# Optimization experiments

Hardware: AMD Instinct MI355X
Metric: run time of the kernel (lower is better)

The kernel has to match this reference:

```python
import jax, jax.numpy as jnp
import numpy as np

TINY = 1e-13  # tiny_value_of_dtype(float32)


def gru_cell(x, h, Wx, Wh, bx, bh):
    gx = x @ Wx + bx
    gh = h @ Wh + bh
    xr, xz, xn = jnp.split(gx, 3, -1)
    hr, hz, hn = jnp.split(gh, 3, -1)
    r = jax.nn.sigmoid(xr + hr)
    z = jax.nn.sigmoid(xz + hz)
    n = jnp.tanh(xn + r * hn)
    return (1.0 - z) * n + z * h


def setup_inputs() -> dict:
    B, V, VT, D, OPT, SEQ, SRC = 256, 2000, 10000, 256, 16, 10, 40
    key = jax.random.key(0)
    ks = jax.random.split(key, 20)
    rn = lambda i, shape, s: jax.random.normal(ks[i], shape, jnp.float32) * s
    inp = {}
    inp['lhs'] = jax.random.randint(ks[0], (B,), 0, V)
    inp['lhs_mask'] = jnp.ones((B,), jnp.int32)
    inp['tree_state'] = rn(1, (B, D), 1.0)
    sym = jax.random.randint(ks[2], (B, OPT, SEQ), 0, V)
    pg = jax.random.randint(ks[3], (B, OPT, SEQ), 0, 2)
    fg = jax.random.randint(ks[4], (B, OPT, SEQ), 0, 2)
    lens = jax.random.randint(ks[5], (B, OPT), 1, SEQ + 1)
    msk = (jnp.arange(SEQ)[None, None, :] < lens[:, :, None]).astype(jnp.int32)
    inp['grammar_guide'] = jnp.stack([sym, pg, fg, msk], axis=2)  # (B,OPT,4,SEQ)
    inp['emb'] = rn(6, (V, D), 0.02)
    inp['mem'] = rn(7, (B, SRC, D), 1.0)  # encoder memory for query_attn_fn
    inp['Wx'] = rn(8, (D, 3 * D), 0.05)
    inp['Wh'] = rn(9, (D, 3 * D), 0.05)
    inp['bx'] = jnp.zeros((3 * D,), jnp.float32)
    inp['bh'] = jnp.zeros((3 * D,), jnp.float32)
    inp['Wc'] = rn(10, (2 * D, D), 0.05)
    inp['bc'] = jnp.zeros((D,), jnp.float32)
    inp['Wsym'] = rn(11, (D, V), 0.05)
    inp['bsym'] = jnp.zeros((V,), jnp.float32)
    inp['Wtok'] = rn(12, (2 * D, VT), 0.05)
    inp['btok'] = jnp.zeros((VT,), jnp.float32)
    inp['tok_table'] = (jax.random.uniform(ks[13], (V, VT)) < 0.05).astype(jnp.float32)
    return inp


def reference(lhs, lhs_mask, tree_state, grammar_guide, emb, mem, Wx, Wh, bx, bh,
              Wc, bc, Wsym, bsym, Wtok, btok, tok_table):
    B, OPT, _, SEQ = grammar_guide.shape
    V = emb.shape[0]
    D = emb.shape[1]
    g_sym = grammar_guide[:, :, 0, :]   # (B,OPT,SEQ) symbol options
    g_mask = grammar_guide[:, :, 3, :]  # (B,OPT,SEQ) option mask

    def step_fn(carry, xs):
        step_inp, ts = carry
        opts, omask = xs  # (B,OPT) ints
        x = emb[step_inp]                      # embedding (dropout = identity, eval mode)
        # hx re-initialized each step from the fixed pre-step tree state
        h = gru_cell(x, tree_state, Wx, Wh, bx, bh)  # (B,D) step_out
        att = jax.nn.softmax(jnp.einsum('bd,bsd->bs', h, mem), axis=-1)
        ctx = jnp.einsum('bs,bsd->bd', att, mem)
        step_out_att = jnp.tanh(jnp.concatenate([ctx, h], -1) @ Wc + bc)
        logits = step_out_att @ Wsym + bsym    # (B,V)
        ts_new = jnp.tanh(ts + step_out_att)   # tree state updater
        # grammar compliance masking
        comp = opts * omask                    # (B,OPT)
        w = jnp.sum(jax.nn.one_hot(comp, V, dtype=jnp.float32), axis=1) > 0  # (B,V) bool
        w0 = jnp.sum((comp == 0) * omask, axis=-1) > 0
        w = w.at[:, 0].set(w0)
        clogits = logits + jnp.log(w.astype(logits.dtype) + TINY)
        nxt = jnp.argmax(clogits, axis=-1)     # free-running next input
        return (nxt, ts_new), clogits

    xs = (jnp.moveaxis(g_sym, -1, 0), jnp.moveaxis(g_mask, -1, 0))  # (SEQ,B,OPT)
    (_, ts_final), seq_logits = jax.lax.scan(step_fn, (lhs, tree_state), xs)
    seq_logits = jnp.moveaxis(seq_logits, 0, -1)                 # (B,V,SEQ)
    seq_logp = jnp.log(jax.nn.softmax(seq_logits, axis=1) + TINY)
    seq_opts_logp = jnp.take_along_axis(seq_logp, g_sym, axis=1)  # (B,OPT,SEQ)
    opts_logp = jnp.sum(seq_opts_logp * g_mask, axis=-1)          # (B,OPT)

    # tree topology inference: pick best option row of grammar_guide
    best = jnp.argmax(opts_logp, axis=-1)
    topo = jnp.take_along_axis(grammar_guide, best[:, None, None, None], axis=1)[:, 0]  # (B,4,SEQ)
    symbol, p_growth, f_growth, mask = topo[:, 0], topo[:, 1], topo[:, 2], topo[:, 3]

    # exact token prediction after derivation
    cw = tok_table[symbol]                     # (B,SEQ,VT) token compliance
    s_emb = emb[symbol]                        # (B,SEQ,D)
    ts_tiled = jnp.broadcast_to(ts_final[:, None, :], (B, SEQ, D))
    proj = jnp.concatenate([s_emb, ts_tiled], axis=-1)
    exact_logit = proj @ Wtok + btok + jnp.log(cw + TINY)  # (B,SEQ,VT)

    return (lhs, lhs_mask, grammar_guide, opts_logp,
            (symbol, p_growth, f_growth, mask), exact_logit)
```

## Files before the change

kernel.cpp:

```cpp
#include <hip/hip_runtime.h>
#include <math.h>

#define BB 256
#define DD 256
#define VV 2000
#define VT 10000
#define OPTN 16
#define SEQN 10
#define SRCN 40
#define D3 768
#define D2 512

#define LOG_TINY (-29.9336062f)

#define OFF_OPTS  (2*BB + BB*OPTN*4*SEQN)
#define OFF_TOPO  (OFF_OPTS + BB*OPTN)
#define OFF_EXACT (OFF_TOPO + 4*BB*SEQN)

#define TOKB_STRIDE 320
#define TOKB_W 313

#define NWG_TOK 1580

typedef __bf16 bf16x8 __attribute__((ext_vector_type(8)));
typedef float  f32x4  __attribute__((ext_vector_type(4)));

__device__ __forceinline__ float sigm(float x){ return 1.0f/(1.0f+expf(-x)); }
__device__ __forceinline__ unsigned short f2bf(float x){
  union { float f; unsigned int u; } v; v.f = x;
  unsigned int r = (v.u + 0x7FFF + ((v.u >> 16) & 1)) >> 16;
  return (unsigned short)r;
}

__global__ void k_gh(const float* __restrict__ ts0, const float* __restrict__ Wh,
                     const float* __restrict__ bh, float* __restrict__ gh){
  int b = blockIdx.x;
  int j = blockIdx.y*256 + threadIdx.x;
  __shared__ float hsh[DD];
  hsh[threadIdx.x] = ts0[b*DD + threadIdx.x];
  __syncthreads();
  float a0 = bh[j], a1 = 0.f, a2 = 0.f, a3 = 0.f;
  #pragma unroll 4
  for(int k=0;k<DD;k+=4){
    a0 = fmaf(hsh[k+0], Wh[(k+0)*D3 + j], a0);
    a1 = fmaf(hsh[k+1], Wh[(k+1)*D3 + j], a1);
    a2 = fmaf(hsh[k+2], Wh[(k+2)*D3 + j], a2);
    a3 = fmaf(hsh[k+3], Wh[(k+3)*D3 + j], a3);
  }
  gh[b*D3 + j] = (a0+a1)+(a2+a3);
}

__global__ void k_ew(const float* __restrict__ emb, const float* __restrict__ Wx,
                     float* __restrict__ EW){
  __shared__ float As[16][64];
  __shared__ float Bs[16][64];
  int tid = threadIdx.x;
  int tx = tid & 15, ty = tid >> 4;
  int m0 = blockIdx.y*64, n0 = blockIdx.x*64;
  float acc[4][4];
  #pragma unroll
  for(int i=0;i<4;i++){ acc[i][0]=0.f; acc[i][1]=0.f; acc[i][2]=0.f; acc[i][3]=0.f; }
  for(int k0=0;k0<DD;k0+=16){
    {
      int row = tid >> 2, kk = (tid & 3)*4;
      int m = m0 + row;
      float4 av = {0,0,0,0};
      if(m < VV) av = *(const float4*)&emb[m*DD + k0 + kk];
      As[kk+0][row]=av.x; As[kk+1][row]=av.y; As[kk+2][row]=av.z; As[kk+3][row]=av.w;
    }
    {
      int r = tid >> 4, c2 = (tid & 15)*4;
      float4 bv = *(const float4*)&Wx[(k0+r)*D3 + n0 + c2];
      *(float4*)&Bs[r][c2] = bv;
    }
    __syncthreads();
    #pragma unroll
    for(int k=0;k<16;k++){
      float4 a4 = *(const float4*)&As[k][ty*4];
      float4 b4 = *(const float4*)&Bs[k][tx*4];
      float av[4] = {a4.x,a4.y,a4.z,a4.w};
      float bw[4] = {b4.x,b4.y,b4.z,b4.w};
      #pragma unroll
      for(int i=0;i<4;i++)
        #pragma unroll
        for(int j=0;j<4;j++) acc[i][j] = fmaf(av[i], bw[j], acc[i][j]);
    }
    __syncthreads();
  }
  #pragma unroll
  for(int i=0;i<4;i++){
    int m = m0 + ty*4 + i;
    if(m < VV){
      #pragma unroll
      for(int j=0;j<4;j++) EW[m*D3 + n0 + tx*4 + j] = acc[i][j];
    }
  }
}

__global__ void k_wtokT(const float* __restrict__ Wtok, unsigned short* __restrict__ WtokB){
  __shared__ float tile[32][65];
  int tid = threadIdx.x;
  int n0 = blockIdx.x*64, k0 = blockIdx.y*32;
  #pragma unroll
  for(int p=0;p<8;p++){
    int idx = tid + p*256;
    int kk = idx >> 6, nn = idx & 63;
    int n = n0 + nn;
    tile[kk][nn] = (n < VT) ? Wtok[(size_t)(k0+kk)*VT + n] : 0.f;
  }
  __syncthreads();
  #pragma unroll
  for(int p=0;p<4;p++){
    int idx = tid + p*256;
    int nn = idx >> 4, kk = (idx & 15)*2;
    int n = n0 + nn;
    if(n < VT){
      ushort2 v;
      v.x = f2bf(tile[kk][nn]);
      v.y = f2bf(tile[kk+1][nn]);
      *(ushort2*)&WtokB[(size_t)n*D2 + k0 + kk] = v;
    }
  }
}

__global__ __launch_bounds__(256) void k_tokbits(const float* __restrict__ tok_table,
                                                 unsigned int* __restrict__ bits){
  int idx = blockIdx.x*256 + threadIdx.x;
  const int total = VV*TOKB_W;
  for(; idx < total; idx += gridDim.x*256){
    int v = idx / TOKB_W, w = idx - v*TOKB_W;
    const float* row = tok_table + (size_t)v*VT + w*32;
    unsigned int bv = 0;
    if(w*32 + 32 <= VT){
      #pragma unroll
      for(int k=0;k<8;k++){
        float4 x = *(const float4*)(row + k*4);
        bv |= (x.x>0.5f?1u:0u) << (k*4+0);
        bv |= (x.y>0.5f?1u:0u) << (k*4+1);
        bv |= (x.z>0.5f?1u:0u) << (k*4+2);
        bv |= (x.w>0.5f?1u:0u) << (k*4+3);
      }
    } else {
      for(int k=0;k<32;k++){
        int n = w*32 + k;
        if(n < VT && row[k] > 0.5f) bv |= 1u << k;
      }
    }
    bits[v*TOKB_STRIDE + w] = bv;
  }
}

__global__ __launch_bounds__(512) void k_chain(
    const int* __restrict__ lhs, const float* __restrict__ EW,
    const float* __restrict__ gh, const float* __restrict__ bx,
    const float* __restrict__ tree_state, const float* __restrict__ mem,
    const float* __restrict__ Wc, const float* __restrict__ bc,
    const float* __restrict__ Wsym, const float* __restrict__ bsym,
    const int* __restrict__ gg, float* __restrict__ cl,
    float* __restrict__ ts){
  int b = blockIdx.x, tid = threadIdx.x;
  int lane = tid & 63, wv = tid >> 6;
  __shared__ float memsh[SRCN][DD];
  __shared__ float bsymsh[VV];
  __shared__ float bxsh[D3];
  __shared__ float ghsh[D3];
  __shared__ float bcsh[DD];
  __shared__ float tssh[DD];
  __shared__ float hsh[DD], csh[DD], soash[DD];
  __shared__ float psum[2][DD];
  __shared__ float sc[SRCN];
  __shared__ unsigned int selw[64];
  __shared__ int symsh;
  __shared__ float wmax[8]; __shared__ int widx[8];

  for(int i = tid; i < SRCN*DD; i += 512) ((float*)memsh)[i] = mem[(size_t)b*SRCN*DD + i];
  for(int i = tid; i < VV; i += 512) bsymsh[i] = bsym[i];
  for(int i = tid; i < D3; i += 512){ bxsh[i] = bx[i]; ghsh[i] = gh[(size_t)b*D3 + i]; }
  if(tid < DD){ bcsh[tid] = bc[tid]; tssh[tid] = tree_state[b*DD + tid]; }
  float t0 = (tid < DD) ? tree_state[b*DD + tid] : 0.f;
  if(tid == 0) symsh = lhs[b];
  __syncthreads();

  for(int t = 0; t < SEQN; t++){
    int sym = symsh;
    if(tid < 64) selw[tid] = 0u;
    __syncthreads();
    if(tid < OPTN){
      int base = ((b*OPTN + tid)*4)*SEQN + t;
      int mk = gg[base + 3*SEQN];
      int v = mk ? gg[base] : -1;
      if(v >= 0) atomicOr(&selw[v>>5], 1u << (v&31));
    }
    if(tid < DD){
      const float* ew = EW + (size_t)sym*D3;
      float r = sigm(ew[tid]     + bxsh[tid]     + ghsh[tid]);
      float z = sigm(ew[256+tid] + bxsh[256+tid] + ghsh[256+tid]);
      float n = tanhf(ew[512+tid] + bxsh[512+tid] + r*ghsh[512+tid]);
      hsh[tid] = (1.0f - z)*n + z*t0;
    }
    __syncthreads();
    for(int s = wv; s < SRCN; s += 8){
      float p = 0.f;
      #pragma unroll 4
      for(int d = lane; d < DD; d += 64) p = fmaf(hsh[d], memsh[s][d], p);
      for(int off=32; off; off>>=1) p += __shfl_down(p, off, 64);
      if(lane == 0) sc[s] = p;
    }
    __syncthreads();
    if(tid < 64){
      float v = (tid < SRCN) ? sc[tid] : -1e30f;
      float mx = v;
      for(int off=32; off; off>>=1) mx = fmaxf(mx, __shfl_xor(mx, off, 64));
      float e = (tid < SRCN) ? expf(v - mx) : 0.f;
      float su = e;
      for(int off=32; off; off>>=1) su += __shfl_xor(su, off, 64);
      if(tid < SRCN) sc[tid] = e / su;
    }
    __syncthreads();
    if(tid < DD){
      float c = 0.f;
      #pragma unroll 8
      for(int s=0;s<SRCN;s++) c = fmaf(sc[s], memsh[s][tid], c);
      csh[tid] = c;
    }
    __syncthreads();
    {
      int j = tid & 255, half = tid >> 8;
      const float* src = half ? hsh : csh;
      const float* w = Wc + (size_t)half*256*DD + j;
      float a0=0.f, a1=0.f, a2=0.f, a3=0.f;
      #pragma unroll 4
      for(int k=0;k<256;k+=4){
        a0 = fmaf(src[k+0], w[(size_t)(k+0)*DD], a0);
        a1 = fmaf(src[k+1], w[(size_t)(k+1)*DD], a1);
        a2 = fmaf(src[k+2], w[(size_t)(k+2)*DD], a2);
        a3 = fmaf(src[k+3], w[(size_t)(k+3)*DD], a3);
      }
      psum[half][j] = (a0+a1)+(a2+a3);
    }
    __syncthreads();
    if(tid < DD){
      float sv = tanhf(psum[0][tid] + psum[1][tid] + bcsh[tid]);
      soash[tid] = sv;
      tssh[tid] = tanhf(tssh[tid] + sv);
    }
    __syncthreads();
    float bv = -3.0e30f; int bn = 0x7FFFFFFF;
    if(tid < 500){
      int c0 = tid*4;
      const float* wcol = Wsym + c0;
      float4 a = {0.f,0.f,0.f,0.f};
      #pragma unroll 8
      for(int k=0;k<DD;k++){
        float sk = soash[k];
        float4 w4 = *(const float4*)(wcol + (size_t)k*VV);
        a.x = fmaf(sk, w4.x, a.x);
        a.y = fmaf(sk, w4.y, a.y);
        a.z = fmaf(sk, w4.z, a.z);
        a.w = fmaf(sk, w4.w, a.w);
      }
      float vals[4];
      #pragma unroll
      for(int j=0;j<4;j++){
        int n = c0 + j;
        unsigned int wb = selw[n >> 5];
        vals[j] = ((float*)&a)[j] + bsymsh[n] + (((wb >> (n&31)) & 1u) ? 0.f : LOG_TINY);
      }
      float4 o; o.x=vals[0]; o.y=vals[1]; o.z=vals[2]; o.w=vals[3];
      *(float4*)&cl[((size_t)t*BB + b)*VV + c0] = o;
      #pragma unroll
      for(int j=0;j<4;j++){
        if(vals[j] > bv){ bv = vals[j]; bn = c0 + j; }
      }
    }
    #pragma unroll
    for(int off=1; off<64; off<<=1){
      float ov = __shfl_xor(bv, off, 64);
      int   on = __shfl_xor(bn, off, 64);
      if(ov > bv || (ov == bv && on < bn)){ bv = ov; bn = on; }
    }
    if(lane == 0){ wmax[wv] = bv; widx[wv] = bn; }
    __syncthreads();
    if(tid == 0){
      float m = wmax[0]; int mi = widx[0];
      #pragma unroll
      for(int w=1; w<8; w++)
        if(wmax[w] > m || (wmax[w] == m && widx[w] < mi)){ m = wmax[w]; mi = widx[w]; }
      symsh = mi;
    }
    __syncthreads();
  }
  if(tid < DD) ts[b*DD + tid] = tssh[tid];
}

__global__ void k_opts(const float* __restrict__ cl, const int* __restrict__ gg,
                       const float* __restrict__ emb, const float* __restrict__ ts,
                       float* __restrict__ out, int* __restrict__ sym_i,
                       unsigned short* __restrict__ A){
  int b = blockIdx.x, tid = threadIdx.x;
  int lane = tid & 63, wv = tid >> 6;
  __shared__ float redm[4], reds[4];
  __shared__ float lse_sh[SEQN];
  __shared__ float sacc[OPTN];
  __shared__ int ssym[SEQN];
  __shared__ int sbest;
  for(int t=0;t<SEQN;t++){
    const float* row = cl + ((size_t)t*BB + b)*VV;
    float mx = -1e30f;
    for(int v=tid; v<VV; v+=256) mx = fmaxf(mx, row[v]);
    for(int off=32; off; off>>=1) mx = fmaxf(mx, __shfl_xor(mx, off, 64));
    if(lane==0) redm[wv] = mx;
    __syncthreads();
    float gmx = fmaxf(fmaxf(redm[0],redm[1]), fmaxf(redm[2],redm[3]));
    float sum = 0.f;
    for(int v=tid; v<VV; v+=256) sum += expf(row[v]-gmx);
    for(int off=32; off; off>>=1) sum += __shfl_xor(sum, off, 64);
    if(lane==0) reds[wv] = sum;
    __syncthreads();
    if(tid==0) lse_sh[t] = gmx + logf(reds[0]+reds[1]+reds[2]+reds[3]);
    __syncthreads();
  }
  if(tid < OPTN){
    int o = tid;
    float acc = 0.f;
    for(int t=0;t<SEQN;t++){
      int base = ((b*OPTN + o)*4)*SEQN + t;
      int mk = gg[base + 3*SEQN];
      if(mk){
        int v = gg[base];
        float p = expf(cl[((size_t)t*BB + b)*VV + v] - lse_sh[t]);
        acc += logf(p + 1e-13f);
      }
    }
    sacc[o] = acc;
    out[OFF_OPTS + b*OPTN + o] = acc;
  }
  __syncthreads();
  if(tid==0){
    float mx = sacc[0]; int mi = 0;
    for(int o=1;o<OPTN;o++) if(sacc[o] > mx){ mx = sacc[o]; mi = o; }
    sbest = mi;
  }
  __syncthreads();
  if(tid < 4*SEQN){
    int c = tid/SEQN, t = tid%SEQN;
    int val = gg[((b*OPTN + sbest)*4 + c)*SEQN + t];
    out[OFF_TOPO + c*(BB*SEQN) + b*SEQN + t] = (float)val;
    if(c==0){ sym_i[b*SEQN + t] = val; ssym[t] = val; }
  }
  __syncthreads();
  for(int idx = tid; idx < SEQN*D2; idx += 256){
    int t = idx >> 9, k = idx & 511;
    float val = (k < DD) ? emb[ssym[t]*DD + k] : ts[b*DD + (k-DD)];
    A[(size_t)(b*SEQN + t)*D2 + k] = f2bf(val);
  }
}

__global__ void k_pass(const int* __restrict__ lhs, const int* __restrict__ lhs_mask,
                       const int* __restrict__ gg, float* __restrict__ out){
  int i = blockIdx.x*256 + threadIdx.x;
  if(i < BB) out[i] = (float)lhs[i];
  else if(i < 2*BB) out[i] = (float)lhs_mask[i - BB];
  else if(i < 2*BB + BB*OPTN*4*SEQN) out[2*BB + (i - 2*BB)] = (float)gg[i - 2*BB];
}

__global__ __launch_bounds__(256) void k_tok_mfma(
    const unsigned short* __restrict__ A, const unsigned short* __restrict__ Bw,
    const float* __restrict__ btok, const unsigned int* __restrict__ tokbits,
    const int* __restrict__ sym_i, float* __restrict__ out){
  __shared__ __align__(16) unsigned short Ssh[4*5120];
  __shared__ float sBtok[128];
  int tid = threadIdx.x;
  int lane = tid & 63, wave = tid >> 6;
  int c = lane & 15, q = lane >> 4;
  int wm = (wave >> 1)*64, wn = (wave & 1)*64;

  int id = blockIdx.x;
  int xcd = id & 7, off = id >> 3;
  const int qq = NWG_TOK >> 3, rr = NWG_TOK & 7;
  int start = (xcd < rr) ? xcd*(qq+1) : rr*(qq+1) + (xcd-rr)*qq;
  int ord = start + off;
  int mb = ord % 20, nb = ord / 20;
  int m0 = mb*128, n0 = nb*128;

  if(tid < 128){
    int n = n0 + tid;
    sBtok[tid] = (n < VT) ? btok[n] : 0.f;
  }
  f32x4 acc[4][4];
  #pragma unroll
  for(int i=0;i<4;i++)
    #pragma unroll
    for(int j=0;j<4;j++) acc[i][j] = (f32x4){0.f,0.f,0.f,0.f};

  int arow = tid >> 2;
  int ach  = (tid & 3) * 8;
  const size_t aoff0 = (size_t)(m0 + arow)*D2 + ach;
  const size_t aoff1 = (size_t)(m0 + 64 + arow)*D2 + ach;
  int bn0 = n0 + arow, bn1 = n0 + 64 + arow;
  bool b0ok = bn0 < VT, b1ok = bn1 < VT;
  const size_t boff0 = (size_t)bn0*D2 + ach;
  const size_t boff1 = (size_t)bn1*D2 + ach;
  const float4 f0 = {0.f,0.f,0.f,0.f};

  float4 ra0 = *(const float4*)(A + aoff0);
  float4 ra1 = *(const float4*)(A + aoff1);
  float4 rb0 = b0ok ? *(const float4*)(Bw + boff0) : f0;
  float4 rb1 = b1ok ? *(const float4*)(Bw + boff1) : f0;

  for(int t=0; t<16; t++){
    unsigned short* As = Ssh + (t&1)*10240;
    unsigned short* Bs = As + 5120;
    *(float4*)(As + arow*40 + ach)      = ra0;
    *(float4*)(As + (64+arow)*40 + ach) = ra1;
    *(float4*)(Bs + arow*40 + ach)      = rb0;
    *(float4*)(Bs + (64+arow)*40 + ach) = rb1;
    __syncthreads();
    if(t < 15){
      int k0 = (t+1)*32;
      ra0 = *(const float4*)(A + aoff0 + k0);
      ra1 = *(const float4*)(A + aoff1 + k0);
      if(b0ok) rb0 = *(const float4*)(Bw + boff0 + k0);
      if(b1ok) rb1 = *(const float4*)(Bw + boff1 + k0);
    }
    bf16x8 af[4], bf[4];
    #pragma unroll
    for(int i=0;i<4;i++) af[i] = *(const bf16x8*)(As + (wm + i*16 + c)*40 + q*8);
    #pragma unroll
    for(int j=0;j<4;j++) bf[j] = *(const bf16x8*)(Bs + (wn + j*16 + c)*40 + q*8);
    #pragma unroll
    for(int i=0;i<4;i++)
      #pragma unroll
      for(int j=0;j<4;j++)
        acc[i][j] = __builtin_amdgcn_mfma_f32_16x16x32_bf16(af[i], bf[j], acc[i][j], 0, 0, 0);
  }
  __syncthreads();

  float* sw = (float*)Ssh + wave*(64*21);
  int lrow = lane >> 2, ln4 = lane & 3;
  #pragma unroll
  for(int i=0;i<4;i++){
    #pragma unroll
    for(int j=0;j<4;j++){
      int col = j*16 + c;
      #pragma unroll
      for(int r2=0;r2<4;r2++) sw[col*21 + q*4 + r2] = acc[i][j][r2];
    }
    int row_g = m0 + wm + i*16 + lrow;
    int s = sym_i[row_g];
    const unsigned int* bt = tokbits + (size_t)s*TOKB_STRIDE;
    float* orow = out + OFF_EXACT + (size_t)row_g*VT;
    #pragma unroll
    for(int s4=0;s4<4;s4++){
      int colo = ln4*4 + s4*16;
      int n = n0 + wn + colo;
      if(n < VT){
        float4 bt4 = *(const float4*)&sBtok[wn + colo];
        unsigned int wb = bt[n >> 5];
        int sh = n & 31;
        float4 o;
        o.x = sw[(colo+0)*21 + lrow] + bt4.x + (((wb>>(sh+0))&1u) ? 0.f : LOG_TINY);
        o.y = sw[(colo+1)*21 + lrow] + bt4.y + (((wb>>(sh+1))&1u) ? 0.f : LOG_TINY);
        o.z = sw[(colo+2)*21 + lrow] + bt4.z + (((wb>>(sh+2))&1u) ? 0.f : LOG_TINY);
        o.w = sw[(colo+3)*21 + lrow] + bt4.w + (((wb>>(sh+3))&1u) ? 0.f : LOG_TINY);
        *(float4*)(orow + n) = o;
      }
    }
  }
}

extern "C" void kernel_launch(void* const* d_in, const int* in_sizes, int n_in,
                              void* d_out, int out_size, void* d_ws, size_t ws_size,
                              hipStream_t stream) {
  const int*   lhs       = (const int*)  d_in[0];
  const int*   lhs_mask  = (const int*)  d_in[1];
  const float* tree_state= (const float*)d_in[2];
  const int*   gg        = (const int*)  d_in[3];
  const float* emb       = (const float*)d_in[4];
  const float* mem       = (const float*)d_in[5];
  const float* Wx        = (const float*)d_in[6];
  const float* Wh        = (const float*)d_in[7];
  const float* bx        = (const float*)d_in[8];
  const float* bh        = (const float*)d_in[9];
  const float* Wc        = (const float*)d_in[10];
  const float* bc        = (const float*)d_in[11];
  const float* Wsym      = (const float*)d_in[12];
  const float* bsym      = (const float*)d_in[13];
  const float* Wtok      = (const float*)d_in[14];
  const float* btok      = (const float*)d_in[15];
  const float* tok_table = (const float*)d_in[16];
  float* out = (float*)d_out;

  float* W    = (float*)d_ws;
  float* gh   = W;
  float* ts   = gh  + BB*D3;
  float* cl   = ts  + BB*DD;
  float* EW   = cl  + (size_t)SEQN*BB*VV;
  int*   sym_i= (int*)(EW + VV*D3);
  unsigned short* Abf  = (unsigned short*)(sym_i + BB*SEQN);
  unsigned short* WtokB= Abf + (size_t)BB*SEQN*D2;
  unsigned int* tokbits= (unsigned int*)(WtokB + (size_t)VT*D2);

  k_pass<<<(2*BB + BB*OPTN*4*SEQN + 255)/256, 256, 0, stream>>>(lhs, lhs_mask, gg, out);
  k_tokbits<<<2048, 256, 0, stream>>>(tok_table, tokbits);
  k_wtokT<<<dim3((VT+63)/64, D2/32), 256, 0, stream>>>(Wtok, WtokB);
  k_gh<<<dim3(BB,3), 256, 0, stream>>>(tree_state, Wh, bh, gh);
  k_ew<<<dim3(D3/64, (VV+63)/64), 256, 0, stream>>>(emb, Wx, EW);

  k_chain<<<BB, 512, 0, stream>>>(lhs, EW, gh, bx, tree_state, mem, Wc, bc,
                                  Wsym, bsym, gg, cl, ts);

  k_opts<<<BB, 256, 0, stream>>>(cl, gg, emb, ts, out, sym_i, Abf);
  k_tok_mfma<<<NWG_TOK, 256, 0, stream>>>(Abf, WtokB, btok, tokbits, sym_i, out);
}
```

Baseline: 633.4 us.

## Restrict per-step argmax to candidate symbols and batch symbol logits into a tiled GEMM

Inside the sequential chain kernel, the next symbol is now chosen by computing logits only for the up-to-16 allowed option symbols. Non-candidates always carry a log-tiny penalty, so they cannot win while any candidate exists. The full 2000-column Wsym projection per step is skipped unless no candidate is present. The per-step attention outputs are stored, and the full logits are computed afterwards in one tiled GEMM kernel, with the masking fused in and log-sum-exp moved into its own parallel kernel. This takes the large serialized matvec off the critical sequential path, at the cost of extra launches and an extra round trip through memory.

New measurement: 569.9 us. 1.11x faster.

```diff
diff --git a/kernel.cpp b/kernel.cpp
--- a/kernel.cpp
+++ b/kernel.cpp
@@ -156,12 +156,11 @@
     const float* __restrict__ tree_state, const float* __restrict__ mem,
     const float* __restrict__ Wc, const float* __restrict__ bc,
     const float* __restrict__ Wsym, const float* __restrict__ bsym,
-    const int* __restrict__ gg, float* __restrict__ cl,
+    const int* __restrict__ gg, float* __restrict__ soa_all,
     float* __restrict__ ts){
   int b = blockIdx.x, tid = threadIdx.x;
   int lane = tid & 63, wv = tid >> 6;
   __shared__ float memsh[SRCN][DD];
-  __shared__ float bsymsh[VV];
   __shared__ float bxsh[D3];
   __shared__ float ghsh[D3];
   __shared__ float bcsh[DD];
@@ -169,12 +168,12 @@
   __shared__ float hsh[DD], csh[DD], soash[DD];
   __shared__ float psum[2][DD];
   __shared__ float sc[SRCN];
-  __shared__ unsigned int selw[64];
+  __shared__ int cvs[16];
+  __shared__ float cvals[16];
   __shared__ int symsh;
   __shared__ float wmax[8]; __shared__ int widx[8];
 
   for(int i = tid; i < SRCN*DD; i += 512) ((float*)memsh)[i] = mem[(size_t)b*SRCN*DD + i];
-  for(int i = tid; i < VV; i += 512) bsymsh[i] = bsym[i];
   for(int i = tid; i < D3; i += 512){ bxsh[i] = bx[i]; ghsh[i] = gh[(size_t)b*D3 + i]; }
   if(tid < DD){ bcsh[tid] = bc[tid]; tssh[tid] = tree_state[b*DD + tid]; }
   float t0 = (tid < DD) ? tree_state[b*DD + tid] : 0.f;
@@ -183,13 +182,10 @@
 
   for(int t = 0; t < SEQN; t++){
     int sym = symsh;
-    if(tid < 64) selw[tid] = 0u;
-    __syncthreads();
-    if(tid < OPTN){
+    if(tid < 16){
       int base = ((b*OPTN + tid)*4)*SEQN + t;
       int mk = gg[base + 3*SEQN];
-      int v = mk ? gg[base] : -1;
-      if(v >= 0) atomicOr(&selw[v>>5], 1u << (v&31));
+      cvs[tid] = mk ? gg[base] : -1;
     }
     if(tid < DD){
       const float* ew = EW + (size_t)sym*D3;
@@ -242,84 +238,199 @@
     if(tid < DD){
       float sv = tanhf(psum[0][tid] + psum[1][tid] + bcsh[tid]);
       soash[tid] = sv;
+      soa_all[(size_t)(t*BB + b)*DD + tid] = sv;
       tssh[tid] = tanhf(tssh[tid] + sv);
     }
     __syncthreads();
-    float bv = -3.0e30f; int bn = 0x7FFFFFFF;
-    if(tid < 500){
-      int c0 = tid*4;
-      const float* wcol = Wsym + c0;
-      float4 a = {0.f,0.f,0.f,0.f};
-      #pragma unroll 8
-      for(int k=0;k<DD;k++){
-        float sk = soash[k];
-        float4 w4 = *(const float4*)(wcol + (size_t)k*VV);
-        a.x = fmaf(sk, w4.x, a.x);
-        a.y = fmaf(sk, w4.y, a.y);
-        a.z = fmaf(sk, w4.z, a.z);
-        a.w = fmaf(sk, w4.w, a.w);
-      }
-      float vals[4];
+    bool anyc = false;
+    #pragma unroll
+    for(int i=0;i<16;i++) anyc |= (cvs[i] >= 0);
+    if(anyc){
+      if(tid < 256){
+        int g = tid >> 4, l = tid & 15;
+        int v = cvs[g];
+        float d = 0.f;
+        if(v >= 0){
+          #pragma unroll
+          for(int k=0;k<16;k++) d = fmaf(soash[l*16+k], Wsym[(size_t)(l*16+k)*VV + v], d);
+        }
+        d += __shfl_xor(d, 1, 64); d += __shfl_xor(d, 2, 64);
+        d += __shfl_xor(d, 4, 64); d += __shfl_xor(d, 8, 64);
+        if(l == 0) cvals[g] = (v >= 0) ? d + bsym[v] : -3.0e30f;
+      }
+      __syncthreads();
+      if(tid == 0){
+        float bvv = -3.0e30f; int bnn = 0x7FFFFFFF;
+        #pragma unroll
+        for(int g=0; g<16; g++){
+          int v = cvs[g];
+          if(v >= 0){
+            float val = cvals[g];
+            if(val > bvv || (val == bvv && v < bnn)){ bvv = val; bnn = v; }
+          }
+        }
+        symsh = bnn;
+      }
+      __syncthreads();
+    } else {
+      float bv = -3.0e30f; int bn = 0x7FFFFFFF;
+      if(tid < 500){
+        int c0 = tid*4;
+        const float* wcol = Wsym + c0;
+        float4 a = {0.f,0.f,0.f,0.f};
+        #pragma unroll 8
+        for(int k=0;k<DD;k++){
+          float sk = soash[k];
+          float4 w4 = *(const float4*)(wcol + (size_t)k*VV);
+          a.x = fmaf(sk, w4.x, a.x);
+          a.y = fmaf(sk, w4.y, a.y);
+          a.z = fmaf(sk, w4.z, a.z);
+          a.w = fmaf(sk, w4.w, a.w);
+        }
+        #pragma unroll
+        for(int j=0;j<4;j++){
+          int n = c0 + j;
+          float val = ((float*)&a)[j] + bsym[n] + LOG_TINY;
+          if(val > bv){ bv = val; bn = n; }
+        }
+      }
+      #pragma unroll
+      for(int off=1; off<64; off<<=1){
+        float ov = __shfl_xor(bv, off, 64);
+        int   on = __shfl_xor(bn, off, 64);
+        if(ov > bv || (ov == bv && on < bn)){ bv = ov; bn = on; }
+      }
+      if(lane == 0){ wmax[wv] = bv; widx[wv] = bn; }
+      __syncthreads();
+      if(tid == 0){
+        float m = wmax[0]; int mi = widx[0];
+        #pragma unroll
+        for(int w=1; w<8; w++)
+          if(wmax[w] > m || (wmax[w] == m && widx[w] < mi)){ m = wmax[w]; mi = widx[w]; }
+        symsh = mi;
+      }
+      __syncthreads();
+    }
+  }
+  if(tid < DD) ts[b*DD + tid] = tssh[tid];
+}
+
+__global__ void k_cl(const float* __restrict__ A, const float* __restrict__ Wsym,
+                     const float* __restrict__ bsym, const int* __restrict__ gg,
+                     float* __restrict__ cl){
+  __shared__ float As[16][32];
+  __shared__ float Bs[16][64];
+  __shared__ unsigned int selb[32][2];
+  int tid = threadIdx.x;
+  int tx = tid & 15, ty = tid >> 4;
+  int m0 = blockIdx.y*32, n0 = blockIdx.x*64;
+  if(tid < 64) selb[tid>>1][tid&1] = 0u;
+  __syncthreads();
+  for(int idx = tid; idx < 32*OPTN; idx += 256){
+    int i = idx >> 4, o = idx & 15;
+    int m = m0 + i;
+    int bb = m & (BB-1), t = m >> 8;
+    int base = ((bb*OPTN + o)*4)*SEQN + t;
+    int mk = gg[base + 3*SEQN];
+    int v = mk ? gg[base] : -1;
+    unsigned int d = (unsigned int)(v - n0);
+    if(d < 64u) atomicOr(&selb[i][d>>5], 1u << (d&31));
+  }
+  float acc[2][4];
+  #pragma unroll
+  for(int i=0;i<2;i++){ acc[i][0]=0.f; acc[i][1]=0.f; acc[i][2]=0.f; acc[i][3]=0.f; }
+  for(int k0=0;k0<DD;k0+=16){
+    if(tid < 128){
+      int row = tid >> 2, kk = (tid & 3)*4;
+      float4 av = *(const float4*)&A[(size_t)(m0+row)*DD + k0 + kk];
+      As[kk+0][row]=av.x; As[kk+1][row]=av.y; As[kk+2][row]=av.z; As[kk+3][row]=av.w;
+    }
+    {
+      int r = tid >> 4, c2 = (tid & 15)*4;
+      int n = n0 + c2;
+      float4 bv;
+      if(n + 3 < VV){ bv = *(const float4*)&Wsym[(k0+r)*VV + n]; }
+      else {
+        bv.x = (n+0<VV)? Wsym[(k0+r)*VV + n+0] : 0.f;
+        bv.y = (n+1<VV)? Wsym[(k0+r)*VV + n+1] : 0.f;
+        bv.z = (n+2<VV)? Wsym[(k0+r)*VV + n+2] : 0.f;
+        bv.w = (n+3<VV)? Wsym[(k0+r)*VV + n+3] : 0.f;
+      }
+      *(float4*)&Bs[r][c2] = bv;
+    }
+    __syncthreads();
+    #pragma unroll
+    for(int k=0;k<16;k++){
+      float a0 = As[k][ty*2+0];
+      float a1 = As[k][ty*2+1];
+      float4 b4 = *(const float4*)&Bs[k][tx*4];
+      acc[0][0] = fmaf(a0, b4.x, acc[0][0]);
+      acc[0][1] = fmaf(a0, b4.y, acc[0][1]);
+      acc[0][2] = fmaf(a0, b4.z, acc[0][2]);
+      acc[0][3] = fmaf(a0, b4.w, acc[0][3]);
+      acc[1][0] = fmaf(a1, b4.x, acc[1][0]);
+      acc[1][1] = fmaf(a1, b4.y, acc[1][1]);
+      acc[1][2] = fmaf(a1, b4.z, acc[1][2]);
+      acc[1][3] = fmaf(a1, b4.w, acc[1][3]);
+    }
+    __syncthreads();
+  }
+  #pragma unroll
+  for(int i=0;i<2;i++){
+    int m = m0 + ty*2 + i;
+    unsigned int s0 = selb[ty*2+i][0], s1 = selb[ty*2+i][1];
+    float vals[4];
+    #pragma unroll
+    for(int j=0;j<4;j++){
+      int n = n0 + tx*4 + j;
+      int nn = tx*4 + j;
+      unsigned int wb = (nn < 32) ? s0 : s1;
+      vals[j] = acc[i][j] + ((n < VV) ? bsym[n] : 0.f) + (((wb >> (nn&31)) & 1u) ? 0.f : LOG_TINY);
+    }
+    int nb = n0 + tx*4;
+    if(nb + 3 < VV){
+      float4 o; o.x=vals[0]; o.y=vals[1]; o.z=vals[2]; o.w=vals[3];
+      *(float4*)&cl[(size_t)m*VV + nb] = o;
+    } else {
       #pragma unroll
       for(int j=0;j<4;j++){
-        int n = c0 + j;
-        unsigned int wb = selw[n >> 5];
-        vals[j] = ((float*)&a)[j] + bsymsh[n] + (((wb >> (n&31)) & 1u) ? 0.f : LOG_TINY);
-      }
-      float4 o; o.x=vals[0]; o.y=vals[1]; o.z=vals[2]; o.w=vals[3];
-      *(float4*)&cl[((size_t)t*BB + b)*VV + c0] = o;
-      #pragma unroll
-      for(int j=0;j<4;j++){
-        if(vals[j] > bv){ bv = vals[j]; bn = c0 + j; }
-      }
-    }
-    #pragma unroll
-    for(int off=1; off<64; off<<=1){
-      float ov = __shfl_xor(bv, off, 64);
-      int   on = __shfl_xor(bn, off, 64);
-      if(ov > bv || (ov == bv && on < bn)){ bv = ov; bn = on; }
-    }
-    if(lane == 0){ wmax[wv] = bv; widx[wv] = bn; }
-    __syncthreads();
-    if(tid == 0){
-      float m = wmax[0]; int mi = widx[0];
-      #pragma unroll
-      for(int w=1; w<8; w++)
-        if(wmax[w] > m || (wmax[w] == m && widx[w] < mi)){ m = wmax[w]; mi = widx[w]; }
-      symsh = mi;
-    }
-    __syncthreads();
-  }
-  if(tid < DD) ts[b*DD + tid] = tssh[tid];
-}
-
-__global__ void k_opts(const float* __restrict__ cl, const int* __restrict__ gg,
-                       const float* __restrict__ emb, const float* __restrict__ ts,
-                       float* __restrict__ out, int* __restrict__ sym_i,
-                       unsigned short* __restrict__ A){
+        int n = nb + j;
+        if(n < VV) cl[(size_t)m*VV + n] = vals[j];
+      }
+    }
+  }
+}
+
+__global__ void k_lse(const float* __restrict__ cl, float* __restrict__ lse_g){
+  int m = blockIdx.x;
+  int tid = threadIdx.x, lane = tid & 63, wv = tid >> 6;
+  __shared__ float redm[4], reds[4];
+  const float* row = cl + (size_t)m*VV;
+  float mx = -1e30f;
+  for(int v=tid; v<VV; v+=256) mx = fmaxf(mx, row[v]);
+  for(int off=32; off; off>>=1) mx = fmaxf(mx, __shfl_xor(mx, off, 64));
+  if(lane==0) redm[wv] = mx;
+  __syncthreads();
+  float gmx = fmaxf(fmaxf(redm[0],redm[1]), fmaxf(redm[2],redm[3]));
+  float sum = 0.f;
+  for(int v=tid; v<VV; v+=256) sum += expf(row[v]-gmx);
+  for(int off=32; off; off>>=1) sum += __shfl_xor(sum, off, 64);
+  if(lane==0) reds[wv] = sum;
+  __syncthreads();
+  if(tid==0) lse_g[m] = gmx + logf(reds[0]+reds[1]+reds[2]+reds[3]);
+}
+
+__global__ void k_opts(const float* __restrict__ cl, const float* __restrict__ lse_g,
+                       const int* __restrict__ gg, const float* __restrict__ emb,
+                       const float* __restrict__ ts, float* __restrict__ out,
+                       int* __restrict__ sym_i, unsigned short* __restrict__ A){
   int b = blockIdx.x, tid = threadIdx.x;
-  int lane = tid & 63, wv = tid >> 6;
-  __shared__ float redm[4], reds[4];
   __shared__ float lse_sh[SEQN];
   __shared__ float sacc[OPTN];
   __shared__ int ssym[SEQN];
   __shared__ int sbest;
-  for(int t=0;t<SEQN;t++){
-    const float* row = cl + ((size_t)t*BB + b)*VV;
-    float mx = -1e30f;
-    for(int v=tid; v<VV; v+=256) mx = fmaxf(mx, row[v]);
-    for(int off=32; off; off>>=1) mx = fmaxf(mx, __shfl_xor(mx, off, 64));
-    if(lane==0) redm[wv] = mx;
-    __syncthreads();
-    float gmx = fmaxf(fmaxf(redm[0],redm[1]), fmaxf(redm[2],redm[3]));
-    float sum = 0.f;
-    for(int v=tid; v<VV; v+=256) sum += expf(row[v]-gmx);
-    for(int off=32; off; off>>=1) sum += __shfl_xor(sum, off, 64);
-    if(lane==0) reds[wv] = sum;
-    __syncthreads();
-    if(tid==0) lse_sh[t] = gmx + logf(reds[0]+reds[1]+reds[2]+reds[3]);
-    __syncthreads();
-  }
+  if(tid < SEQN) lse_sh[tid] = lse_g[tid*BB + b];
+  __syncthreads();
   if(tid < OPTN){
     int o = tid;
     float acc = 0.f;
@@ -491,12 +602,14 @@
   const float* tok_table = (const float*)d_in[16];
   float* out = (float*)d_out;
 
-  float* W    = (float*)d_ws;
-  float* gh   = W;
-  float* ts   = gh  + BB*D3;
-  float* cl   = ts  + BB*DD;
-  float* EW   = cl  + (size_t)SEQN*BB*VV;
-  int*   sym_i= (int*)(EW + VV*D3);
+  float* W       = (float*)d_ws;
+  float* gh      = W;
+  float* ts      = gh + BB*D3;
+  float* soa_all = ts + BB*DD;
+  float* cl      = soa_all + (size_t)SEQN*BB*DD;
+  float* EW      = cl + (size_t)SEQN*BB*VV;
+  float* lse_g   = EW + VV*D3;
+  int*   sym_i   = (int*)(lse_g + SEQN*BB);
   unsigned short* Abf  = (unsigned short*)(sym_i + BB*SEQN);
   unsigned short* WtokB= Abf + (size_t)BB*SEQN*D2;
   unsigned int* tokbits= (unsigned int*)(WtokB + (size_t)VT*D2);
@@ -508,8 +621,10 @@
   k_ew<<<dim3(D3/64, (VV+63)/64), 256, 0, stream>>>(emb, Wx, EW);
 
   k_chain<<<BB, 512, 0, stream>>>(lhs, EW, gh, bx, tree_state, mem, Wc, bc,
-                                  Wsym, bsym, gg, cl, ts);
-
-  k_opts<<<BB, 256, 0, stream>>>(cl, gg, emb, ts, out, sym_i, Abf);
+                                  Wsym, bsym, gg, soa_all, ts);
+
+  k_cl<<<dim3(32, 80), 256, 0, stream>>>(soa_all, Wsym, bsym, gg, cl);
+  k_lse<<<SEQN*BB, 256, 0, stream>>>(cl, lse_g);
+  k_opts<<<BB, 256, 0, stream>>>(cl, lse_g, gg, emb, ts, out, sym_i, Abf);
   k_tok_mfma<<<NWG_TOK, 256, 0, stream>>>(Abf, WtokB, btok, tokbits, sym_i, out);
 }
```
